# Performance work log

Hardware: AMD Instinct MI355X
Metric: run time of the kernel (lower is better)

## Reference

```python
import jax, jax.numpy as jnp
import numpy as np

B, T, D, H = 2048, 2048, 3, 32  # batch, time steps, input_size, hidden_size


def setup_inputs() -> dict:
    key = jax.random.key(0)
    k0, k1, k2, k3, k4 = jax.random.split(key, 5)
    lim = 1.0 / np.sqrt(H)  # eqx.nn.GRUCell init range
    inp = jax.random.normal(k0, (B, T, D), dtype=jnp.float32)
    weight_ih = jax.random.uniform(k1, (3 * H, D), minval=-lim, maxval=lim, dtype=jnp.float32)
    weight_hh = jax.random.uniform(k2, (3 * H, H), minval=-lim, maxval=lim, dtype=jnp.float32)
    bias = jax.random.uniform(k3, (3 * H,), minval=-lim, maxval=lim, dtype=jnp.float32)
    bias_n = jax.random.uniform(k4, (H,), minval=-lim, maxval=lim, dtype=jnp.float32)
    return {"inp": inp, "weight_ih": weight_ih, "weight_hh": weight_hh,
            "bias": bias, "bias_n": bias_n}


def reference(inp, weight_ih, weight_hh, bias, bias_n):
    # inp: [B, T, D]. Faithful batched version of PinnWithGRU.__call__:
    # scan an eqx.nn.GRUCell over time from a zero hidden state, output hidden[0] per step.
    b = inp.shape[0]
    h0 = jnp.zeros((b, H), dtype=inp.dtype)
    xs = jnp.swapaxes(inp, 0, 1)  # [T, B, D]

    def step(h, x):
        ig = x @ weight_ih.T + bias      # [B, 3H] input gates (+ bias, as in eqx)
        hg = h @ weight_hh.T             # [B, 3H] hidden gates
        ir, iz, ia = jnp.split(ig, 3, axis=-1)
        hr, hz, ha = jnp.split(hg, 3, axis=-1)
        r = jax.nn.sigmoid(ir + hr)
        z = jax.nn.sigmoid(iz + hz)
        n = jnp.tanh(ia + bias_n + r * ha)
        h_new = (1.0 - z) * n + z * h
        return h_new, h_new[:, 0]        # emit first hidden unit per step

    _, out = jax.lax.scan(step, h0, xs)  # out: [T, B]
    return jnp.swapaxes(out, 0, 1)[..., None]  # [B, T, 1] (matches per-seq [T, 1])
```

## Files before the change

### kernel.cpp

```cpp
#include <hip/hip_runtime.h>


#define GRU_B 2048
#define GRU_T 2048
#define GRU_D 3
#define GRU_H 32
#define CHUNK 32

#define WAIT_LGKM0 0xC07F

__device__ __forceinline__ float fast_sigmoid(float x) {
    float e = __expf(-x);
    return __builtin_amdgcn_rcpf(1.0f + e);
}
__device__ __forceinline__ float fast_tanh(float x) {
    float e = __expf(2.0f * x);
    return 1.0f - 2.0f * __builtin_amdgcn_rcpf(e + 1.0f);
}
__device__ __forceinline__ float xor32(float v, int paddr) {
    return __int_as_float(__builtin_amdgcn_ds_bpermute(paddr, __float_as_int(v)));
}

__global__ __launch_bounds__(64, 2) void gru_scan_kernel(
    const float* __restrict__ inp,
    const float* __restrict__ w_ih,
    const float* __restrict__ w_hh,
    const float* __restrict__ bias,
    const float* __restrict__ bias_n,
    float* __restrict__ out)
{
    __shared__ __align__(16) float h2[4 * GRU_H];
    __shared__ __align__(16) float x_lds[CHUNK * GRU_D];

    const int lane  = threadIdx.x;
    const int unit  = lane & 31;
    const int half  = lane >> 5;
    const int b     = blockIdx.x;
    const int paddr = (lane ^ 32) << 2;

    const int rowA = unit + 32 * half;
    const int rowB = unit + 32 * (1 - half);
    const int rowC = 2 * GRU_H + unit;
    const int kofs = 16 * half;

    float wa[16], wb[16], wc[16];
    {
        const float4* pa = (const float4*)(w_hh + (size_t)rowA * GRU_H + kofs);
        const float4* pb = (const float4*)(w_hh + (size_t)rowB * GRU_H + kofs);
        const float4* pc = (const float4*)(w_hh + (size_t)rowC * GRU_H + kofs);
#pragma unroll
        for (int q = 0; q < 4; ++q) {
            float4 A = pa[q], Bv = pb[q], Cv = pc[q];
            wa[4*q+0]=A.x;  wa[4*q+1]=A.y;  wa[4*q+2]=A.z;  wa[4*q+3]=A.w;
            wb[4*q+0]=Bv.x; wb[4*q+1]=Bv.y; wb[4*q+2]=Bv.z; wb[4*q+3]=Bv.w;
            wc[4*q+0]=Cv.x; wc[4*q+1]=Cv.y; wc[4*q+2]=Cv.z; wc[4*q+3]=Cv.w;
        }
    }
    float wia[GRU_D], wic[GRU_D];
#pragma unroll
    for (int d = 0; d < GRU_D; ++d) {
        wia[d] = w_ih[(size_t)rowA * GRU_D + d];
        wic[d] = w_ih[(size_t)rowC * GRU_D + d];
    }
    const float bA = bias[rowA];
    const float bC = bias[rowC] + bias_n[unit];

    const float* xb = inp + (size_t)b * GRU_T * GRU_D;
    float*       ob = out + (size_t)b * GRU_T;

    float h = 0.0f;
    float outreg = 0.0f;

    h2[lane] = 0.0f;
    __builtin_amdgcn_s_waitcnt(WAIT_LGKM0);

    const float4* hv = (const float4*)(h2 + 48 * half);
    const int wbase = unit + 64 * half;

    for (int c = 0; c < GRU_T / CHUNK; ++c) {
        {
            const int base = c * (CHUNK * GRU_D);
            x_lds[lane] = xb[base + lane];
            if (lane < CHUNK * GRU_D - 64) x_lds[64 + lane] = xb[base + 64 + lane];
        }
        __builtin_amdgcn_s_waitcnt(WAIT_LGKM0);

#pragma unroll 8
        for (int s = 0; s < CHUNK; ++s) {
            float hk[16];
#pragma unroll
            for (int q = 0; q < 4; ++q) {
                float4 v = hv[q];
                hk[4*q+0]=v.x; hk[4*q+1]=v.y; hk[4*q+2]=v.z; hk[4*q+3]=v.w;
            }
            const float x0 = x_lds[3 * s + 0];
            const float x1 = x_lds[3 * s + 1];
            const float x2 = x_lds[3 * s + 2];

            const float aM = fmaf(wia[2], x2, fmaf(wia[1], x1, fmaf(wia[0], x0, bA)));
            const float aN = fmaf(wic[2], x2, fmaf(wic[1], x1, fmaf(wic[0], x0, bC)));

            float A = 0.0f, Bp = 0.0f, Cp = 0.0f;
#pragma unroll
            for (int k = 0; k < 16; ++k) {
                A  = fmaf(wa[k], hk[k], A);
                Bp = fmaf(wb[k], hk[k], Bp);
                Cp = fmaf(wc[k], hk[k], Cp);
            }
            const float gM = A  + xor32(Bp, paddr);
            const float gN = Cp + xor32(Cp, paddr);

            const float sg  = fast_sigmoid(aM + gM);
            const float zsw = xor32(sg, paddr);
            const float n   = fast_tanh(fmaf(sg, gN, aN));
            const float hnew = fmaf(zsw, h - n, n);

            if (lane == s - 1) outreg = hk[0];

            h = hnew;
            h2[wbase]      = h;
            h2[wbase + 32] = h;
            __builtin_amdgcn_s_waitcnt(WAIT_LGKM0);
        }

        {
            const float h0 = h2[0];
            if (lane == CHUNK - 1) outreg = h0;
        }
        if (lane < CHUNK) ob[c * CHUNK + lane] = outreg;
    }
}

extern "C" void kernel_launch(void* const* d_in, const int* in_sizes, int n_in,
                              void* d_out, int out_size, void* d_ws, size_t ws_size,
                              hipStream_t stream) {
    const float* inp    = (const float*)d_in[0];
    const float* w_ih   = (const float*)d_in[1];
    const float* w_hh   = (const float*)d_in[2];
    const float* bias   = (const float*)d_in[3];
    const float* bias_n = (const float*)d_in[4];
    float* out = (float*)d_out;

    dim3 grid(GRU_B);
    dim3 block(64);
    gru_scan_kernel<<<grid, block, 0, stream>>>(inp, w_ih, w_hh, bias, bias_n, out);
}
```

Before: 708.6 us.

## Map one sequence per half-wave with full hidden dot products per lane

Each 64-lane block now processes two batch sequences, one per 32-lane half. Each lane holds the full r, z and n weight rows (96 registers) and computes the complete 32-wide dot products itself. This removes the ds_bpermute cross-half exchanges and the explicit LDS waitcnts from the serial step chain. Inputs are read straight from global memory each step instead of being staged in LDS. The cost is twice the FMAs per lane, higher register pressure, half as many blocks in the grid, and less latency hiding from other waves.

```diff
diff --git a/kernel.cpp b/kernel.cpp
--- a/kernel.cpp
+++ b/kernel.cpp
@@ -17,11 +17,8 @@
     float e = __expf(2.0f * x);
     return 1.0f - 2.0f * __builtin_amdgcn_rcpf(e + 1.0f);
 }
-__device__ __forceinline__ float xor32(float v, int paddr) {
-    return __int_as_float(__builtin_amdgcn_ds_bpermute(paddr, __float_as_int(v)));
-}
 
-__global__ __launch_bounds__(64, 2) void gru_scan_kernel(
+__global__ __launch_bounds__(64, 1) void gru_scan_kernel(
     const float* __restrict__ inp,
     const float* __restrict__ w_ih,
     const float* __restrict__ w_hh,
@@ -29,105 +26,90 @@
     const float* __restrict__ bias_n,
     float* __restrict__ out)
 {
-    __shared__ __align__(16) float h2[4 * GRU_H];
-    __shared__ __align__(16) float x_lds[CHUNK * GRU_D];
+    __shared__ __align__(16) float h2[80];
 
-    const int lane  = threadIdx.x;
-    const int unit  = lane & 31;
-    const int half  = lane >> 5;
-    const int b     = blockIdx.x;
-    const int paddr = (lane ^ 32) << 2;
+    const int lane = threadIdx.x;
+    const int p    = lane & 31;
+    const int hf   = lane >> 5;
+    const size_t seq = 2 * (size_t)blockIdx.x + hf;
 
-    const int rowA = unit + 32 * half;
-    const int rowB = unit + 32 * (1 - half);
-    const int rowC = 2 * GRU_H + unit;
-    const int kofs = 16 * half;
-
-    float wa[16], wb[16], wc[16];
+    float wr[32], wz[32], wn[32];
     {
-        const float4* pa = (const float4*)(w_hh + (size_t)rowA * GRU_H + kofs);
-        const float4* pb = (const float4*)(w_hh + (size_t)rowB * GRU_H + kofs);
-        const float4* pc = (const float4*)(w_hh + (size_t)rowC * GRU_H + kofs);
+        const float4* pr = (const float4*)(w_hh + (size_t)p * GRU_H);
+        const float4* pz = (const float4*)(w_hh + (size_t)(GRU_H + p) * GRU_H);
+        const float4* pn = (const float4*)(w_hh + (size_t)(2 * GRU_H + p) * GRU_H);
 #pragma unroll
-        for (int q = 0; q < 4; ++q) {
-            float4 A = pa[q], Bv = pb[q], Cv = pc[q];
-            wa[4*q+0]=A.x;  wa[4*q+1]=A.y;  wa[4*q+2]=A.z;  wa[4*q+3]=A.w;
-            wb[4*q+0]=Bv.x; wb[4*q+1]=Bv.y; wb[4*q+2]=Bv.z; wb[4*q+3]=Bv.w;
-            wc[4*q+0]=Cv.x; wc[4*q+1]=Cv.y; wc[4*q+2]=Cv.z; wc[4*q+3]=Cv.w;
+        for (int q = 0; q < 8; ++q) {
+            float4 R = pr[q], Z = pz[q], N = pn[q];
+            wr[4*q+0]=R.x; wr[4*q+1]=R.y; wr[4*q+2]=R.z; wr[4*q+3]=R.w;
+            wz[4*q+0]=Z.x; wz[4*q+1]=Z.y; wz[4*q+2]=Z.z; wz[4*q+3]=Z.w;
+            wn[4*q+0]=N.x; wn[4*q+1]=N.y; wn[4*q+2]=N.z; wn[4*q+3]=N.w;
         }
     }
-    float wia[GRU_D], wic[GRU_D];
+    float wir[GRU_D], wiz[GRU_D], win[GRU_D];
 #pragma unroll
     for (int d = 0; d < GRU_D; ++d) {
-        wia[d] = w_ih[(size_t)rowA * GRU_D + d];
-        wic[d] = w_ih[(size_t)rowC * GRU_D + d];
+        wir[d] = w_ih[(size_t)p * GRU_D + d];
+        wiz[d] = w_ih[(size_t)(GRU_H + p) * GRU_D + d];
+        win[d] = w_ih[(size_t)(2 * GRU_H + p) * GRU_D + d];
     }
-    const float bA = bias[rowA];
-    const float bC = bias[rowC] + bias_n[unit];
+    const float bR = bias[p];
+    const float bZ = bias[GRU_H + p];
+    const float bN = bias[2 * GRU_H + p] + bias_n[p];
 
-    const float* xb = inp + (size_t)b * GRU_T * GRU_D;
-    float*       ob = out + (size_t)b * GRU_T;
+    const float* xp = inp + seq * (size_t)(GRU_T * GRU_D);
+    float*       ob = out + seq * (size_t)GRU_T;
+
+    const int hbase = 48 * hf;
+    float* hw = h2 + hbase + p;
+    const float4* hv = (const float4*)(h2 + hbase);
 
     float h = 0.0f;
-    float outreg = 0.0f;
-
-    h2[lane] = 0.0f;
-    __builtin_amdgcn_s_waitcnt(WAIT_LGKM0);
-
-    const float4* hv = (const float4*)(h2 + 48 * half);
-    const int wbase = unit + 64 * half;
+    *hw = 0.0f;
 
     for (int c = 0; c < GRU_T / CHUNK; ++c) {
-        {
-            const int base = c * (CHUNK * GRU_D);
-            x_lds[lane] = xb[base + lane];
-            if (lane < CHUNK * GRU_D - 64) x_lds[64 + lane] = xb[base + 64 + lane];
-        }
-        __builtin_amdgcn_s_waitcnt(WAIT_LGKM0);
-
+        float outreg = 0.0f;
 #pragma unroll 8
         for (int s = 0; s < CHUNK; ++s) {
-            float hk[16];
+            const int t = c * CHUNK + s;
+            const float x0 = xp[3 * t + 0];
+            const float x1 = xp[3 * t + 1];
+            const float x2 = xp[3 * t + 2];
+
+            float4 hk[8];
 #pragma unroll
-            for (int q = 0; q < 4; ++q) {
-                float4 v = hv[q];
-                hk[4*q+0]=v.x; hk[4*q+1]=v.y; hk[4*q+2]=v.z; hk[4*q+3]=v.w;
+            for (int q = 0; q < 8; ++q) hk[q] = hv[q];
+
+            const float aR = fmaf(wir[2], x2, fmaf(wir[1], x1, fmaf(wir[0], x0, bR)));
+            const float aZ = fmaf(wiz[2], x2, fmaf(wiz[1], x1, fmaf(wiz[0], x0, bZ)));
+            const float aN = fmaf(win[2], x2, fmaf(win[1], x1, fmaf(win[0], x0, bN)));
+
+            float r0=0.f, r1=0.f, z0=0.f, z1=0.f, n0=0.f, n1=0.f;
+#pragma unroll
+            for (int q = 0; q < 8; ++q) {
+                const float4 v = hk[q];
+                r0 = fmaf(wr[4*q+0], v.x, r0); r1 = fmaf(wr[4*q+1], v.y, r1);
+                r0 = fmaf(wr[4*q+2], v.z, r0); r1 = fmaf(wr[4*q+3], v.w, r1);
+                z0 = fmaf(wz[4*q+0], v.x, z0); z1 = fmaf(wz[4*q+1], v.y, z1);
+                z0 = fmaf(wz[4*q+2], v.z, z0); z1 = fmaf(wz[4*q+3], v.w, z1);
+                n0 = fmaf(wn[4*q+0], v.x, n0); n1 = fmaf(wn[4*q+1], v.y, n1);
+                n0 = fmaf(wn[4*q+2], v.z, n0); n1 = fmaf(wn[4*q+3], v.w, n1);
             }
-            const float x0 = x_lds[3 * s + 0];
-            const float x1 = x_lds[3 * s + 1];
-            const float x2 = x_lds[3 * s + 2];
+            const float rg = fast_sigmoid(aR + (r0 + r1));
+            const float zg = fast_sigmoid(aZ + (z0 + z1));
+            const float ng = fast_tanh(fmaf(rg, n0 + n1, aN));
+            const float hnew = fmaf(zg, h - ng, ng);
 
-            const float aM = fmaf(wia[2], x2, fmaf(wia[1], x1, fmaf(wia[0], x0, bA)));
-            const float aN = fmaf(wic[2], x2, fmaf(wic[1], x1, fmaf(wic[0], x0, bC)));
-
-            float A = 0.0f, Bp = 0.0f, Cp = 0.0f;
-#pragma unroll
-            for (int k = 0; k < 16; ++k) {
-                A  = fmaf(wa[k], hk[k], A);
-                Bp = fmaf(wb[k], hk[k], Bp);
-                Cp = fmaf(wc[k], hk[k], Cp);
-            }
-            const float gM = A  + xor32(Bp, paddr);
-            const float gN = Cp + xor32(Cp, paddr);
-
-            const float sg  = fast_sigmoid(aM + gM);
-            const float zsw = xor32(sg, paddr);
-            const float n   = fast_tanh(fmaf(sg, gN, aN));
-            const float hnew = fmaf(zsw, h - n, n);
-
-            if (lane == s - 1) outreg = hk[0];
+            if (p == s - 1) outreg = hk[0].x;
 
             h = hnew;
-            h2[wbase]      = h;
-            h2[wbase + 32] = h;
-            __builtin_amdgcn_s_waitcnt(WAIT_LGKM0);
+            *hw = h;
         }
-
         {
-            const float h0 = h2[0];
-            if (lane == CHUNK - 1) outreg = h0;
+            const float h0 = h2[hbase];
+            if (p == CHUNK - 1) outreg = h0;
         }
-        if (lane < CHUNK) ob[c * CHUNK + lane] = outreg;
+        ob[c * CHUNK + p] = outreg;
     }
 }
 
@@ -141,7 +123,7 @@
     const float* bias_n = (const float*)d_in[4];
     float* out = (float*)d_out;
 
-    dim3 grid(GRU_B);
+    dim3 grid(GRU_B / 2);
     dim3 block(64);
     gru_scan_kernel<<<grid, block, 0, stream>>>(inp, w_ih, w_hh, bias, bias_n, out);
 }
```

New measurement: 640.7 us. -9.6%, faster.
